# Kernel tuning notes

Measured on AMD Instinct MI355X. Metric: run time of the kernel, lower is better.

Reference implementation:

```python
import jax, jax.numpy as jnp
import numpy as np

N, E, F_IN, HID, L, G = 50000, 400000, 128, 64, 3, 512
HEADS = 4  # per-head dim C = HID = 64 (PyG TransformerConv: out_channels per head)


def setup_inputs() -> dict:
    key = jax.random.key(0)
    ks = jax.random.split(key, 16)
    x = jax.random.normal(ks[0], (N, F_IN), dtype=jnp.float32)
    edge_index = jax.random.randint(ks[1], (2, E), 0, N, dtype=jnp.int64)
    batch = jnp.sort(jax.random.randint(ks[2], (N,), 0, G, dtype=jnp.int64))
    s_in = 1.0 / np.sqrt(F_IN)
    s_h = 1.0 / np.sqrt(HID)
    lin0_w = jax.random.normal(ks[3], (F_IN, HID), dtype=jnp.float32) * s_in
    lin0_b = jnp.zeros((HID,), dtype=jnp.float32)
    # stacked per-layer params [L, ...]
    Wq = jax.random.normal(ks[4], (L, HID, HEADS * HID), dtype=jnp.float32) * s_h
    Wk = jax.random.normal(ks[5], (L, HID, HEADS * HID), dtype=jnp.float32) * s_h
    Wv = jax.random.normal(ks[6], (L, HID, HEADS * HID), dtype=jnp.float32) * s_h
    bq = jnp.zeros((L, HEADS * HID), dtype=jnp.float32)
    bk = jnp.zeros((L, HEADS * HID), dtype=jnp.float32)
    bv = jnp.zeros((L, HEADS * HID), dtype=jnp.float32)
    Ws = jax.random.normal(ks[7], (L, HID, HID), dtype=jnp.float32) * s_h
    bs = jnp.zeros((L, HID), dtype=jnp.float32)
    return {"x": x, "edge_index": edge_index, "batch": batch,
            "lin0_w": lin0_w, "lin0_b": lin0_b,
            "Wq": Wq, "bq": bq, "Wk": Wk, "bk": bk, "Wv": Wv, "bv": bv,
            "Ws": Ws, "bs": bs}


def _transformer_conv(h, src, dst, Wq, bq, Wk, bk, Wv, bv, Ws, bs):
    n = h.shape[0]
    C = Wq.shape[1] // HEADS
    q = (h @ Wq + bq).reshape(n, HEADS, C)
    k = (h @ Wk + bk).reshape(n, HEADS, C)
    v = (h @ Wv + bv).reshape(n, HEADS, C)
    # per-edge attention logits: query at dst, key at src  -> [E, H]
    scale = jnp.asarray(1.0 / np.sqrt(C), h.dtype)
    logits = jnp.einsum('ehc,ehc->eh', q[dst], k[src]) * scale
    # segment softmax over incoming edges of each destination node
    m = jax.ops.segment_max(logits, dst, num_segments=n)
    e = jnp.exp(logits - m[dst])
    denom = jax.ops.segment_sum(e, dst, num_segments=n)
    p = e / denom[dst]  # every edge's dst segment is nonempty
    agg = jax.ops.segment_sum(p[:, :, None] * v[src], dst, num_segments=n)  # [n,H,C]
    return agg.mean(axis=1) + h @ Ws + bs  # concat=False: head mean + root skip


def reference(x, edge_index, batch, lin0_w, lin0_b, Wq, bq, Wk, bk, Wv, bv, Ws, bs):
    src, dst = edge_index[0], edge_index[1]
    h = x @ lin0_w + lin0_b  # [N, HID]; dropout is identity in eval mode
    for l in range(L):
        h = jax.nn.relu(_transformer_conv(h, src, dst, Wq[l], bq[l], Wk[l], bk[l],
                                          Wv[l], bv[l], Ws[l], bs[l]))
    # global add pool over graphs
    return jax.ops.segment_sum(h, batch, num_segments=G)  # [G, HID]
```

## Files before the change

kernel.cpp:

```cpp
#include <hip/hip_runtime.h>
#include <math.h>

#define F_IN 128
#define HID 64
#define NLAYER 3
#define QSW 832
#define QS_ROW 320
#define KV_ROW 512

typedef unsigned short ushort_t;
typedef __bf16 bf16x8 __attribute__((ext_vector_type(8)));
typedef unsigned short u16x8 __attribute__((ext_vector_type(8)));
typedef float f32x4 __attribute__((ext_vector_type(4)));
typedef float f32x2 __attribute__((ext_vector_type(2)));

__device__ __forceinline__ ushort_t f2bf(float f) {
  unsigned u = __float_as_uint(f);
  u += 0x7fffu + ((u >> 16) & 1u);
  return (ushort_t)(u >> 16);
}
__device__ __forceinline__ float bf2f(ushort_t s) {
  return __uint_as_float(((unsigned)s) << 16);
}
__device__ __forceinline__ float blo(unsigned u) { return __uint_as_float(u << 16); }
__device__ __forceinline__ float bhi(unsigned u) { return __uint_as_float(u & 0xffff0000u); }

__device__ __forceinline__ void dec8(uint2 u, float* f) {
  f32x2 a0 = __builtin_amdgcn_cvt_pk_f32_fp8((int)u.x, false);
  f32x2 a1 = __builtin_amdgcn_cvt_pk_f32_fp8((int)u.x, true);
  f32x2 a2 = __builtin_amdgcn_cvt_pk_f32_fp8((int)u.y, false);
  f32x2 a3 = __builtin_amdgcn_cvt_pk_f32_fp8((int)u.y, true);
  f[0] = a0[0]; f[1] = a0[1]; f[2] = a1[0]; f[3] = a1[1];
  f[4] = a2[0]; f[5] = a2[1]; f[6] = a3[0]; f[7] = a3[1];
}

__global__ __launch_bounds__(256) void hist_k(const int* __restrict__ dst, int* __restrict__ cnt, int e) {
  int i = blockIdx.x * 256 + threadIdx.x;
  if (i < e) atomicAdd(&cnt[dst[i]], 1);
}
__global__ __launch_bounds__(1024) void scan_block_k(const int* __restrict__ cnt, int* __restrict__ excl,
                                                     int* __restrict__ bsum, int n) {
  __shared__ int tmp[1024];
  int t = threadIdx.x;
  int i = blockIdx.x * 1024 + t;
  int v = (i < n) ? cnt[i] : 0;
  tmp[t] = v;
  __syncthreads();
  for (int off = 1; off < 1024; off <<= 1) {
    int add = (t >= off) ? tmp[t - off] : 0;
    __syncthreads();
    tmp[t] += add;
    __syncthreads();
  }
  if (i < n) excl[i] = tmp[t] - v;
  if (t == 1023) bsum[blockIdx.x] = tmp[1023];
}
__global__ __launch_bounds__(64) void scan_bsum_k(int* __restrict__ bsum, int nb) {
  int l = threadIdx.x;
  int orig = (l < nb) ? bsum[l] : 0;
  int v = orig;
  for (int off = 1; off < 64; off <<= 1) {
    int u = __shfl_up(v, off);
    if (l >= off) v += u;
  }
  if (l < nb) bsum[l] = v - orig;
}
__global__ __launch_bounds__(256) void scatter_rowptr_k(const int* __restrict__ src, const int* __restrict__ dst,
                                                        const int* __restrict__ excl, const int* __restrict__ bsum,
                                                        int* __restrict__ cur, int* __restrict__ rowp,
                                                        int* __restrict__ srt, int n, int e) {
  int i = blockIdx.x * 256 + threadIdx.x;
  if (i < n) rowp[i] = excl[i] + bsum[i >> 10];
  if (i == 0) rowp[n] = e;
  if (i < e) {
    int d = dst[i];
    int pos = excl[d] + bsum[d >> 10] + atomicAdd(&cur[d], 1);
    srt[pos] = src[i];
  }
}

__global__ __launch_bounds__(64) void pack2_k(const float* __restrict__ Wq, const float* __restrict__ Wk,
                                              const float* __restrict__ Wv, const float* __restrict__ Ws,
                                              const float* __restrict__ w0, const float* __restrict__ b0,
                                              const float* __restrict__ bq, const float* __restrict__ bk,
                                              const float* __restrict__ bv, const float* __restrict__ bs,
                                              ushort_t* __restrict__ wp0, ushort_t* __restrict__ wp12,
                                              float* __restrict__ bp) {
  int b = blockIdx.x, lane = threadIdx.x;
  if (b < 208) {
    int ntg = b >> 2, kt = b & 3;
    int col = ntg * 16 + (lane & 15);
    int kb = kt * 32 + (lane >> 4) * 8;
    const float* W; int c, stride;
    if (col < 256)      { W = Wq; c = col;       stride = 256; }
    else if (col < 512) { W = Wk; c = col - 256; stride = 256; }
    else if (col < 768) { W = Wv; c = col - 512; stride = 256; }
    else                { W = Ws; c = col - 768; stride = 64; }
    float vals[8] = {0.f, 0.f, 0.f, 0.f, 0.f, 0.f, 0.f, 0.f};
    for (int j = 0; j < 64; j++) {
      float wj = W[(long long)j * stride + c];
#pragma unroll
      for (int e = 0; e < 8; e++) vals[e] = fmaf(w0[(kb + e) * 64 + j], wj, vals[e]);
    }
    ushort_t* p = wp0 + ((long long)b * 64 + lane) * 8;
    ushort4 lo{f2bf(vals[0]), f2bf(vals[1]), f2bf(vals[2]), f2bf(vals[3])};
    ushort4 hi{f2bf(vals[4]), f2bf(vals[5]), f2bf(vals[6]), f2bf(vals[7])};
    *(ushort4*)p = lo;
    *(ushort4*)(p + 4) = hi;
  } else if (b < 416) {
    int idx = b - 208;
    int l = 1 + idx / 104, t = idx % 104;
    int ntg = t >> 1, kt = t & 1;
    int col = ntg * 16 + (lane & 15);
    int kb = kt * 32 + (lane >> 4) * 8;
    const float* W; int c, stride;
    if (col < 256)      { W = Wq + (long long)l * 64 * 256; c = col;       stride = 256; }
    else if (col < 512) { W = Wk + (long long)l * 64 * 256; c = col - 256; stride = 256; }
    else if (col < 768) { W = Wv + (long long)l * 64 * 256; c = col - 512; stride = 256; }
    else                { W = Ws + (long long)l * 64 * 64;  c = col - 768; stride = 64; }
    float vals[8];
#pragma unroll
    for (int e = 0; e < 8; e++) vals[e] = W[(long long)(kb + e) * stride + c];
    ushort_t* p = wp12 + (long long)(l - 1) * (104 * 512) + ((long long)t * 64 + lane) * 8;
    ushort4 lo{f2bf(vals[0]), f2bf(vals[1]), f2bf(vals[2]), f2bf(vals[3])};
    ushort4 hi{f2bf(vals[4]), f2bf(vals[5]), f2bf(vals[6]), f2bf(vals[7])};
    *(ushort4*)p = lo;
    *(ushort4*)(p + 4) = hi;
  } else {
    int l = b - 416;
    if (l == 0) {
      for (int c = lane; c < QSW; c += 64) {
        const float* W; const float* borig; int cc, stride;
        if (c < 256)      { W = Wq; borig = bq; cc = c;       stride = 256; }
        else if (c < 512) { W = Wk; borig = bk; cc = c - 256; stride = 256; }
        else if (c < 768) { W = Wv; borig = bv; cc = c - 512; stride = 256; }
        else              { W = Ws; borig = bs; cc = c - 768; stride = 64; }
        float acc = borig[cc];
        for (int j = 0; j < 64; j++) acc = fmaf(b0[j], W[(long long)j * stride + cc], acc);
        bp[c] = acc;
      }
    } else {
      for (int c = lane; c < QSW; c += 64) {
        float v = (c < 256) ? bq[l * 256 + c]
                : (c < 512) ? bk[l * 256 + c - 256]
                : (c < 768) ? bv[l * 256 + c - 512]
                : bs[l * 64 + c - 768];
        bp[l * QSW + c] = v;
      }
    }
  }
}

#define QS_STR 328
#define KV_STR 528
template <int K, int AF32>
__global__ __launch_bounds__(256) void gemm_fused(const void* __restrict__ Av, const ushort_t* __restrict__ Wp,
                                                  const float* __restrict__ bias, ushort_t* __restrict__ Cq,
                                                  unsigned char* __restrict__ Ckv, int n) {
  constexpr int KT = K / 32;
  __shared__ ushort_t qs_lds[32][QS_STR];
  __shared__ unsigned char kv_lds[32][KV_STR];
  int tid = threadIdx.x;
  int lane = tid & 63;
  int wv = __builtin_amdgcn_readfirstlane((int)(tid >> 6));
  int m0 = blockIdx.x * 32;
  int lr = lane & 15, lq = lane >> 4;

  bf16x8 a[2][KT];
#pragma unroll
  for (int mr = 0; mr < 2; mr++) {
    int row = m0 + mr * 16 + lr;
    if (row >= n) row = n - 1;
    if constexpr (AF32) {
      const float* Af = (const float*)Av;
#pragma unroll
      for (int kt = 0; kt < KT; kt++) {
        const float* p = Af + (long long)row * K + kt * 32 + lq * 8;
        float4 f0 = *(const float4*)p;
        float4 f1 = *(const float4*)(p + 4);
        u16x8 u;
        u[0] = f2bf(f0.x); u[1] = f2bf(f0.y); u[2] = f2bf(f0.z); u[3] = f2bf(f0.w);
        u[4] = f2bf(f1.x); u[5] = f2bf(f1.y); u[6] = f2bf(f1.z); u[7] = f2bf(f1.w);
        a[mr][kt] = __builtin_bit_cast(bf16x8, u);
      }
    } else {
      const ushort_t* Ab = (const ushort_t*)Av;
#pragma unroll
      for (int kt = 0; kt < KT; kt++)
        a[mr][kt] = *(const bf16x8*)(Ab + (long long)row * K + kt * 32 + lq * 8);
    }
  }
#pragma unroll 1
  for (int t = 0; t < 13; t++) {
    int ntg = wv * 13 + t;
    float4 b4 = *(const float4*)(bias + ntg * 16 + lq * 4);
    f32x4 acc0 = {b4.x, b4.y, b4.z, b4.w};
    f32x4 acc1 = acc0;
    bf16x8 bw[KT];
#pragma unroll
    for (int kt = 0; kt < KT; kt++)
      bw[kt] = *(const bf16x8*)(Wp + ((long long)(ntg * KT + kt) * 64 + lane) * 8);
#pragma unroll
    for (int kt = 0; kt < KT; kt++) {
      acc0 = __builtin_amdgcn_mfma_f32_16x16x32_bf16(bw[kt], a[0][kt], acc0, 0, 0, 0);
      acc1 = __builtin_amdgcn_mfma_f32_16x16x32_bf16(bw[kt], a[1][kt], acc1, 0, 0, 0);
    }
    if (ntg < 16) {
      int c = ntg * 16 + lq * 4;
      ushort4 o0{f2bf(acc0[0]), f2bf(acc0[1]), f2bf(acc0[2]), f2bf(acc0[3])};
      ushort4 o1{f2bf(acc1[0]), f2bf(acc1[1]), f2bf(acc1[2]), f2bf(acc1[3])};
      *(ushort4*)&qs_lds[lr][c] = o0;
      *(ushort4*)&qs_lds[16 + lr][c] = o1;
    } else if (ntg < 48) {
      int c = ntg * 16 - 256 + lq * 4;
      int p0 = __builtin_amdgcn_cvt_pk_fp8_f32(acc0[0], acc0[1], 0, false);
      p0 = __builtin_amdgcn_cvt_pk_fp8_f32(acc0[2], acc0[3], p0, true);
      int p1 = __builtin_amdgcn_cvt_pk_fp8_f32(acc1[0], acc1[1], 0, false);
      p1 = __builtin_amdgcn_cvt_pk_fp8_f32(acc1[2], acc1[3], p1, true);
      *(unsigned*)&kv_lds[lr][c] = (unsigned)p0;
      *(unsigned*)&kv_lds[16 + lr][c] = (unsigned)p1;
    } else {
      int c = 256 + (ntg - 48) * 16 + lq * 4;
      ushort4 o0{f2bf(acc0[0]), f2bf(acc0[1]), f2bf(acc0[2]), f2bf(acc0[3])};
      ushort4 o1{f2bf(acc1[0]), f2bf(acc1[1]), f2bf(acc1[2]), f2bf(acc1[3])};
      *(ushort4*)&qs_lds[lr][c] = o0;
      *(ushort4*)&qs_lds[16 + lr][c] = o1;
    }
  }
  __syncthreads();
  int rows_here = n - m0;
  if (rows_here > 32) rows_here = 32;
  const char* qsl = (const char*)qs_lds;
  char* qout = (char*)Cq + (long long)m0 * (QS_ROW * 2);
#pragma unroll 1
  for (int off = tid * 16; off < 32 * 640; off += 4096) {
    int row = off / 640;
    if (row >= rows_here) break;
    int col = off - row * 640;
    uint4 v = *(const uint4*)(qsl + row * (QS_STR * 2) + col);
    *(uint4*)(qout + off) = v;
  }
  const char* kvl = (const char*)kv_lds;
  char* kout = (char*)Ckv + (long long)m0 * KV_ROW;
#pragma unroll 1
  for (int off = tid * 16; off < 32 * 512; off += 4096) {
    int row = off >> 9;
    if (row >= rows_here) break;
    int col = off & 511;
    uint4 v = *(const uint4*)(kvl + row * KV_STR + col);
    *(uint4*)(kout + off) = v;
  }
}

__global__ __launch_bounds__(256) void attn_k(const ushort_t* __restrict__ qs,
                                              const unsigned char* __restrict__ kv,
                                              const int* __restrict__ rowp, const int* __restrict__ srt,
                                              ushort_t* __restrict__ hn, int n) {
  int wvv = __builtin_amdgcn_readfirstlane((int)(threadIdx.x >> 6));
  int node = blockIdx.x * 4 + wvv;
  if (node >= n) return;
  int lane = threadIdx.x & 63;
  int half = lane >> 5;
  int sl = lane & 31;
  const uint4 qu = *(const uint4*)(qs + (long long)node * QS_ROW + sl * 8);
  float qf[8];
  qf[0] = blo(qu.x); qf[1] = bhi(qu.x); qf[2] = blo(qu.y); qf[3] = bhi(qu.y);
  qf[4] = blo(qu.z); qf[5] = bhi(qu.z); qf[6] = blo(qu.w); qf[7] = bhi(qu.w);
  int rs = rowp[node], re = rowp[node + 1];
  int last = re - 1;
  float m = -INFINITY, d = 0.f;
  float a[8];
#pragma unroll
  for (int j = 0; j < 8; j++) a[j] = 0.f;

  for (int i = rs; i < re; i += 8) {
    int b0 = i + half * 4;
    int j0 = min(b0, last), j1 = min(b0 + 1, last), j2 = min(b0 + 2, last), j3 = min(b0 + 3, last);
    int i0 = srt[j0], i1 = srt[j1], i2 = srt[j2], i3 = srt[j3];
    const unsigned char* p0 = kv + (long long)i0 * KV_ROW + sl * 8;
    const unsigned char* p1 = kv + (long long)i1 * KV_ROW + sl * 8;
    const unsigned char* p2 = kv + (long long)i2 * KV_ROW + sl * 8;
    const unsigned char* p3 = kv + (long long)i3 * KV_ROW + sl * 8;
    uint2 k0 = *(const uint2*)p0;
    uint2 k1 = *(const uint2*)p1;
    uint2 k2 = *(const uint2*)p2;
    uint2 k3 = *(const uint2*)p3;
    uint2 v0 = *(const uint2*)(p0 + 256);
    uint2 v1 = *(const uint2*)(p1 + 256);
    uint2 v2 = *(const uint2*)(p2 + 256);
    uint2 v3 = *(const uint2*)(p3 + 256);
    float kf0[8], kf1[8], kf2[8], kf3[8];
    dec8(k0, kf0); dec8(k1, kf1); dec8(k2, kf2); dec8(k3, kf3);
    float t0 = 0.f, t1 = 0.f, t2 = 0.f, t3 = 0.f;
#pragma unroll
    for (int j = 0; j < 8; j++) {
      t0 = fmaf(qf[j], kf0[j], t0);
      t1 = fmaf(qf[j], kf1[j], t1);
      t2 = fmaf(qf[j], kf2[j], t2);
      t3 = fmaf(qf[j], kf3[j], t3);
    }
    t0 += __shfl_xor(t0, 1); t1 += __shfl_xor(t1, 1); t2 += __shfl_xor(t2, 1); t3 += __shfl_xor(t3, 1);
    t0 += __shfl_xor(t0, 2); t1 += __shfl_xor(t1, 2); t2 += __shfl_xor(t2, 2); t3 += __shfl_xor(t3, 2);
    t0 += __shfl_xor(t0, 4); t1 += __shfl_xor(t1, 4); t2 += __shfl_xor(t2, 4); t3 += __shfl_xor(t3, 4);
    t0 *= 0.125f; t1 *= 0.125f; t2 *= 0.125f; t3 *= 0.125f;
    if (b0 > last) t0 = -INFINITY;
    if (b0 + 1 > last) t1 = -INFINITY;
    if (b0 + 2 > last) t2 = -INFINITY;
    if (b0 + 3 > last) t3 = -INFINITY;
    float lm = fmaxf(fmaxf(t0, t1), fmaxf(t2, t3));
    lm = fmaxf(lm, __shfl_xor(lm, 32));
    if (__any(lm > m + 8.f)) {
      float mn = fmaxf(m, lm);
      float co = __expf(m - mn);
      d *= co;
#pragma unroll
      for (int j = 0; j < 8; j++) a[j] *= co;
      m = mn;
    }
    float p0e = __expf(t0 - m), p1e = __expf(t1 - m), p2e = __expf(t2 - m), p3e = __expf(t3 - m);
    d += (p0e + p1e) + (p2e + p3e);
    float vf0[8], vf1[8], vf2[8], vf3[8];
    dec8(v0, vf0); dec8(v1, vf1); dec8(v2, vf2); dec8(v3, vf3);
#pragma unroll
    for (int j = 0; j < 8; j++)
      a[j] += fmaf(p0e, vf0[j], p1e * vf1[j]) + fmaf(p2e, vf2[j], p3e * vf3[j]);
  }
  d += __shfl_xor(d, 32);
#pragma unroll
  for (int j = 0; j < 8; j++) a[j] += __shfl_xor(a[j], 32);
  float inv = (d > 0.f) ? 1.f / d : 0.f;
  float r[8];
#pragma unroll
  for (int j = 0; j < 8; j++) {
    r[j] = a[j] * inv;
    r[j] += __shfl_xor(r[j], 8);
    r[j] += __shfl_xor(r[j], 16);
  }
  if (lane < 8) {
    const u16x8 s8 = *(const u16x8*)(qs + (long long)node * QS_ROW + 256 + lane * 8);
    u16x8 o;
#pragma unroll
    for (int j = 0; j < 8; j++)
      o[j] = f2bf(fmaxf(r[j] * 0.25f + bf2f(s8[j]), 0.f));
    *(u16x8*)(hn + (long long)node * HID + lane * 8) = o;
  }
}

#define POOL_NPB 128
__global__ __launch_bounds__(64) void pool_k(const ushort_t* __restrict__ h, const int* __restrict__ batch,
                                             float* __restrict__ out, int n) {
  int c = threadIdx.x;
  int n0 = blockIdx.x * POOL_NPB;
  int n1 = n0 + POOL_NPB;
  if (n1 > n) n1 = n;
  if (n0 >= n) return;
  float acc = 0.f;
  int g = batch[n0];
  for (int node = n0; node < n1; node++) {
    int gb = batch[node];
    if (gb != g) {
      atomicAdd(&out[g * 64 + c], acc);
      acc = 0.f;
      g = gb;
    }
    acc += bf2f(h[(long long)node * 64 + c]);
  }
  atomicAdd(&out[g * 64 + c], acc);
}

extern "C" void kernel_launch(void* const* d_in, const int* in_sizes, int n_in,
                              void* d_out, int out_size, void* d_ws, size_t ws_size,
                              hipStream_t stream) {
  const float* x  = (const float*)d_in[0];
  const int* ei   = (const int*)d_in[1];
  const int* batch = (const int*)d_in[2];
  const float* w0 = (const float*)d_in[3];
  const float* b0 = (const float*)d_in[4];
  const float* Wq = (const float*)d_in[5];
  const float* bq = (const float*)d_in[6];
  const float* Wk = (const float*)d_in[7];
  const float* bk = (const float*)d_in[8];
  const float* Wv = (const float*)d_in[9];
  const float* bv = (const float*)d_in[10];
  const float* Ws = (const float*)d_in[11];
  const float* bs = (const float*)d_in[12];
  int N = in_sizes[0] / F_IN;
  int E = in_sizes[1] / 2;
  const int* esrc = ei;
  const int* edst = ei + E;

  float* bp = (float*)d_ws;
  unsigned char* kvb = (unsigned char*)(bp + 3 * QSW);
  ushort_t* ha = (ushort_t*)(kvb + (size_t)N * KV_ROW);
  ushort_t* hb = ha + (long long)N * HID;
  ushort_t* qs = hb + (long long)N * HID;
  ushort_t* wp0  = qs + (long long)N * QS_ROW;
  ushort_t* wp12 = wp0 + 208 * 512;
  int* cnt  = (int*)(wp12 + 2 * 104 * 512);
  int* cur  = cnt + N;
  int* excl = cur + N;
  int* rowp = excl + N;
  int* bsum = rowp + N + 1;
  int* srt  = bsum + 64;

  int nbE = (E + 255) / 256;
  int sbBlocks = (N + 1023) / 1024;

  hipMemsetAsync(cnt, 0, (size_t)2 * N * sizeof(int), stream);
  hist_k<<<nbE, 256, 0, stream>>>(edst, cnt, E);
  scan_block_k<<<sbBlocks, 1024, 0, stream>>>(cnt, excl, bsum, N);
  scan_bsum_k<<<1, 64, 0, stream>>>(bsum, sbBlocks);
  scatter_rowptr_k<<<nbE, 256, 0, stream>>>(esrc, edst, excl, bsum, cur, rowp, srt, N, E);

  pack2_k<<<419, 64, 0, stream>>>(Wq, Wk, Wv, Ws, w0, b0, bq, bk, bv, bs, wp0, wp12, bp);

  int gBlocks = (N + 31) / 32;

  gemm_fused<128, 1><<<gBlocks, 256, 0, stream>>>(x, wp0, bp, qs, kvb, N);
  attn_k<<<(N + 3) / 4, 256, 0, stream>>>(qs, kvb, rowp, srt, ha, N);
  gemm_fused<64, 0><<<gBlocks, 256, 0, stream>>>(ha, wp12, bp + QSW, qs, kvb, N);
  attn_k<<<(N + 3) / 4, 256, 0, stream>>>(qs, kvb, rowp, srt, hb, N);
  gemm_fused<64, 0><<<gBlocks, 256, 0, stream>>>(hb, wp12 + 104 * 512, bp + 2 * QSW, qs, kvb, N);
  attn_k<<<(N + 3) / 4, 256, 0, stream>>>(qs, kvb, rowp, srt, ha, N);

  hipMemsetAsync(d_out, 0, (size_t)out_size * sizeof(float), stream);
  pool_k<<<(N + POOL_NPB - 1) / POOL_NPB, 64, 0, stream>>>(ha, batch, (float*)d_out, N);
}
```

Baseline: 337.7 us.

## Interleave K/V fp8 rows, prefetch GEMM weights, packed-math attention loop

The projection epilogue now writes K and V fp8 bytes interleaved in 8-byte chunks per row, so the attention kernel fetches each neighbour's K and V slice with a single 16-byte load instead of two 8-byte loads. The GEMM loop prefetches the next tile's weights and bias into registers to overlap global loads with MFMA. The attention loop folds the 1/sqrt(C) scale into q, uses f32x2 vector math so the compiler can emit packed FMAs, and clamps neighbour indices read from srt rather than clamping edge positions. The last change can read srt past the segment end, which relies on padding or valid memory beyond the array.

```diff
diff --git a/kernel.cpp b/kernel.cpp
--- a/kernel.cpp
+++ b/kernel.cpp
@@ -25,13 +25,11 @@
 __device__ __forceinline__ float blo(unsigned u) { return __uint_as_float(u << 16); }
 __device__ __forceinline__ float bhi(unsigned u) { return __uint_as_float(u & 0xffff0000u); }
 
-__device__ __forceinline__ void dec8(uint2 u, float* f) {
-  f32x2 a0 = __builtin_amdgcn_cvt_pk_f32_fp8((int)u.x, false);
-  f32x2 a1 = __builtin_amdgcn_cvt_pk_f32_fp8((int)u.x, true);
-  f32x2 a2 = __builtin_amdgcn_cvt_pk_f32_fp8((int)u.y, false);
-  f32x2 a3 = __builtin_amdgcn_cvt_pk_f32_fp8((int)u.y, true);
-  f[0] = a0[0]; f[1] = a0[1]; f[2] = a1[0]; f[3] = a1[1];
-  f[4] = a2[0]; f[5] = a2[1]; f[6] = a3[0]; f[7] = a3[1];
+__device__ __forceinline__ void dec8v(unsigned lo, unsigned hi, f32x2* f) {
+  f[0] = __builtin_amdgcn_cvt_pk_f32_fp8((int)lo, false);
+  f[1] = __builtin_amdgcn_cvt_pk_f32_fp8((int)lo, true);
+  f[2] = __builtin_amdgcn_cvt_pk_f32_fp8((int)hi, false);
+  f[3] = __builtin_amdgcn_cvt_pk_f32_fp8((int)hi, true);
 }
 
 __global__ __launch_bounds__(256) void hist_k(const int* __restrict__ dst, int* __restrict__ cnt, int e) {
@@ -190,16 +188,25 @@
         a[mr][kt] = *(const bf16x8*)(Ab + (long long)row * K + kt * 32 + lq * 8);
     }
   }
+  int ntg0 = wv * 13;
+  bf16x8 bw[KT];
+#pragma unroll
+  for (int kt = 0; kt < KT; kt++)
+    bw[kt] = *(const bf16x8*)(Wp + ((long long)(ntg0 * KT + kt) * 64 + lane) * 8);
+  float4 b4 = *(const float4*)(bias + ntg0 * 16 + lq * 4);
 #pragma unroll 1
   for (int t = 0; t < 13; t++) {
-    int ntg = wv * 13 + t;
-    float4 b4 = *(const float4*)(bias + ntg * 16 + lq * 4);
+    int ntg = ntg0 + t;
+    bf16x8 bwn[KT];
+    float4 b4n;
+    if (t < 12) {
+#pragma unroll
+      for (int kt = 0; kt < KT; kt++)
+        bwn[kt] = *(const bf16x8*)(Wp + ((long long)((ntg + 1) * KT + kt) * 64 + lane) * 8);
+      b4n = *(const float4*)(bias + (ntg + 1) * 16 + lq * 4);
+    }
     f32x4 acc0 = {b4.x, b4.y, b4.z, b4.w};
     f32x4 acc1 = acc0;
-    bf16x8 bw[KT];
-#pragma unroll
-    for (int kt = 0; kt < KT; kt++)
-      bw[kt] = *(const bf16x8*)(Wp + ((long long)(ntg * KT + kt) * 64 + lane) * 8);
 #pragma unroll
     for (int kt = 0; kt < KT; kt++) {
       acc0 = __builtin_amdgcn_mfma_f32_16x16x32_bf16(bw[kt], a[0][kt], acc0, 0, 0, 0);
@@ -212,13 +219,15 @@
       *(ushort4*)&qs_lds[lr][c] = o0;
       *(ushort4*)&qs_lds[16 + lr][c] = o1;
     } else if (ntg < 48) {
-      int c = ntg * 16 - 256 + lq * 4;
+      bool isK = ntg < 32;
+      int c = (isK ? (ntg - 16) : (ntg - 32)) * 16 + lq * 4;
+      int pos = ((c >> 3) << 4) + (isK ? 0 : 8) + (c & 7);
       int p0 = __builtin_amdgcn_cvt_pk_fp8_f32(acc0[0], acc0[1], 0, false);
       p0 = __builtin_amdgcn_cvt_pk_fp8_f32(acc0[2], acc0[3], p0, true);
       int p1 = __builtin_amdgcn_cvt_pk_fp8_f32(acc1[0], acc1[1], 0, false);
       p1 = __builtin_amdgcn_cvt_pk_fp8_f32(acc1[2], acc1[3], p1, true);
-      *(unsigned*)&kv_lds[lr][c] = (unsigned)p0;
-      *(unsigned*)&kv_lds[16 + lr][c] = (unsigned)p1;
+      *(unsigned*)&kv_lds[lr][pos] = (unsigned)p0;
+      *(unsigned*)&kv_lds[16 + lr][pos] = (unsigned)p1;
     } else {
       int c = 256 + (ntg - 48) * 16 + lq * 4;
       ushort4 o0{f2bf(acc0[0]), f2bf(acc0[1]), f2bf(acc0[2]), f2bf(acc0[3])};
@@ -226,6 +235,9 @@
       *(ushort4*)&qs_lds[lr][c] = o0;
       *(ushort4*)&qs_lds[16 + lr][c] = o1;
     }
+#pragma unroll
+    for (int kt = 0; kt < KT; kt++) bw[kt] = bwn[kt];
+    b4 = b4n;
   }
   __syncthreads();
   int rows_here = n - m0;
@@ -263,46 +275,44 @@
   int half = lane >> 5;
   int sl = lane & 31;
   const uint4 qu = *(const uint4*)(qs + (long long)node * QS_ROW + sl * 8);
-  float qf[8];
-  qf[0] = blo(qu.x); qf[1] = bhi(qu.x); qf[2] = blo(qu.y); qf[3] = bhi(qu.y);
-  qf[4] = blo(qu.z); qf[5] = bhi(qu.z); qf[6] = blo(qu.w); qf[7] = bhi(qu.w);
+  f32x2 qf[4];
+  qf[0] = f32x2{blo(qu.x), bhi(qu.x)} * 0.125f;
+  qf[1] = f32x2{blo(qu.y), bhi(qu.y)} * 0.125f;
+  qf[2] = f32x2{blo(qu.z), bhi(qu.z)} * 0.125f;
+  qf[3] = f32x2{blo(qu.w), bhi(qu.w)} * 0.125f;
   int rs = rowp[node], re = rowp[node + 1];
   int last = re - 1;
+  unsigned nm1 = (unsigned)(n - 1);
   float m = -INFINITY, d = 0.f;
-  float a[8];
-#pragma unroll
-  for (int j = 0; j < 8; j++) a[j] = 0.f;
+  f32x2 a2[4];
+#pragma unroll
+  for (int j = 0; j < 4; j++) a2[j] = f32x2{0.f, 0.f};
 
   for (int i = rs; i < re; i += 8) {
     int b0 = i + half * 4;
-    int j0 = min(b0, last), j1 = min(b0 + 1, last), j2 = min(b0 + 2, last), j3 = min(b0 + 3, last);
-    int i0 = srt[j0], i1 = srt[j1], i2 = srt[j2], i3 = srt[j3];
-    const unsigned char* p0 = kv + (long long)i0 * KV_ROW + sl * 8;
-    const unsigned char* p1 = kv + (long long)i1 * KV_ROW + sl * 8;
-    const unsigned char* p2 = kv + (long long)i2 * KV_ROW + sl * 8;
-    const unsigned char* p3 = kv + (long long)i3 * KV_ROW + sl * 8;
-    uint2 k0 = *(const uint2*)p0;
-    uint2 k1 = *(const uint2*)p1;
-    uint2 k2 = *(const uint2*)p2;
-    uint2 k3 = *(const uint2*)p3;
-    uint2 v0 = *(const uint2*)(p0 + 256);
-    uint2 v1 = *(const uint2*)(p1 + 256);
-    uint2 v2 = *(const uint2*)(p2 + 256);
-    uint2 v3 = *(const uint2*)(p3 + 256);
-    float kf0[8], kf1[8], kf2[8], kf3[8];
-    dec8(k0, kf0); dec8(k1, kf1); dec8(k2, kf2); dec8(k3, kf3);
-    float t0 = 0.f, t1 = 0.f, t2 = 0.f, t3 = 0.f;
-#pragma unroll
-    for (int j = 0; j < 8; j++) {
-      t0 = fmaf(qf[j], kf0[j], t0);
-      t1 = fmaf(qf[j], kf1[j], t1);
-      t2 = fmaf(qf[j], kf2[j], t2);
-      t3 = fmaf(qf[j], kf3[j], t3);
-    }
+    unsigned i0 = min((unsigned)srt[b0], nm1);
+    unsigned i1 = min((unsigned)srt[b0 + 1], nm1);
+    unsigned i2 = min((unsigned)srt[b0 + 2], nm1);
+    unsigned i3 = min((unsigned)srt[b0 + 3], nm1);
+    uint4 u0 = *(const uint4*)(kv + (long long)i0 * KV_ROW + sl * 16);
+    uint4 u1 = *(const uint4*)(kv + (long long)i1 * KV_ROW + sl * 16);
+    uint4 u2 = *(const uint4*)(kv + (long long)i2 * KV_ROW + sl * 16);
+    uint4 u3 = *(const uint4*)(kv + (long long)i3 * KV_ROW + sl * 16);
+    f32x2 kf0[4], kf1[4], kf2[4], kf3[4];
+    dec8v(u0.x, u0.y, kf0); dec8v(u1.x, u1.y, kf1);
+    dec8v(u2.x, u2.y, kf2); dec8v(u3.x, u3.y, kf3);
+    f32x2 s0 = qf[0] * kf0[0], s1 = qf[0] * kf1[0], s2 = qf[0] * kf2[0], s3 = qf[0] * kf3[0];
+#pragma unroll
+    for (int j = 1; j < 4; j++) {
+      s0 = s0 + qf[j] * kf0[j];
+      s1 = s1 + qf[j] * kf1[j];
+      s2 = s2 + qf[j] * kf2[j];
+      s3 = s3 + qf[j] * kf3[j];
+    }
+    float t0 = s0[0] + s0[1], t1 = s1[0] + s1[1], t2 = s2[0] + s2[1], t3 = s3[0] + s3[1];
     t0 += __shfl_xor(t0, 1); t1 += __shfl_xor(t1, 1); t2 += __shfl_xor(t2, 1); t3 += __shfl_xor(t3, 1);
     t0 += __shfl_xor(t0, 2); t1 += __shfl_xor(t1, 2); t2 += __shfl_xor(t2, 2); t3 += __shfl_xor(t3, 2);
     t0 += __shfl_xor(t0, 4); t1 += __shfl_xor(t1, 4); t2 += __shfl_xor(t2, 4); t3 += __shfl_xor(t3, 4);
-    t0 *= 0.125f; t1 *= 0.125f; t2 *= 0.125f; t3 *= 0.125f;
     if (b0 > last) t0 = -INFINITY;
     if (b0 + 1 > last) t1 = -INFINITY;
     if (b0 + 2 > last) t2 = -INFINITY;
@@ -314,20 +324,26 @@
       float co = __expf(m - mn);
       d *= co;
 #pragma unroll
-      for (int j = 0; j < 8; j++) a[j] *= co;
+      for (int j = 0; j < 4; j++) a2[j] = a2[j] * co;
       m = mn;
     }
     float p0e = __expf(t0 - m), p1e = __expf(t1 - m), p2e = __expf(t2 - m), p3e = __expf(t3 - m);
     d += (p0e + p1e) + (p2e + p3e);
-    float vf0[8], vf1[8], vf2[8], vf3[8];
-    dec8(v0, vf0); dec8(v1, vf1); dec8(v2, vf2); dec8(v3, vf3);
-#pragma unroll
-    for (int j = 0; j < 8; j++)
-      a[j] += fmaf(p0e, vf0[j], p1e * vf1[j]) + fmaf(p2e, vf2[j], p3e * vf3[j]);
+    f32x2 vf0[4], vf1[4], vf2[4], vf3[4];
+    dec8v(u0.z, u0.w, vf0); dec8v(u1.z, u1.w, vf1);
+    dec8v(u2.z, u2.w, vf2); dec8v(u3.z, u3.w, vf3);
+    f32x2 pe0 = {p0e, p0e}, pe1 = {p1e, p1e}, pe2 = {p2e, p2e}, pe3 = {p3e, p3e};
+#pragma unroll
+    for (int j = 0; j < 4; j++)
+      a2[j] = a2[j] + (pe0 * vf0[j] + pe1 * vf1[j]) + (pe2 * vf2[j] + pe3 * vf3[j]);
   }
   d += __shfl_xor(d, 32);
-#pragma unroll
-  for (int j = 0; j < 8; j++) a[j] += __shfl_xor(a[j], 32);
+  float a[8];
+#pragma unroll
+  for (int j = 0; j < 4; j++) {
+    a[2 * j] = a2[j][0] + __shfl_xor(a2[j][0], 32);
+    a[2 * j + 1] = a2[j][1] + __shfl_xor(a2[j][1], 32);
+  }
   float inv = (d > 0.f) ? 1.f / d : 0.f;
   float r[8];
 #pragma unroll
```

Result: faster. 328.5 us (-2.7%).
